# Kernel tuning notes

Measured on AMD Instinct MI355X. Metric: run time of the kernel, lower is better.

The kernel has to match this reference:

```python
import jax, jax.numpy as jnp
import numpy as np
import math

N_ATOMS = 128
BATCH = 8
FEAT = 64
K_BASIS = 16
N_IRR = 9            # (max_degree+1)^2 with max_degree=2
CUTOFF = 5.0
N_ELEM = 119
SQ3 = 1.7320508075688772

# degree of each of the 9 irrep components: l = 0,1,1,1,2,2,2,2,2
DEG = np.array([0, 1, 1, 1, 2, 2, 2, 2, 2])
_BINOM = jnp.asarray([math.comb(K_BASIS - 1, k) for k in range(K_BASIS)], dtype=jnp.float32)
_KPOW = jnp.arange(K_BASIS, dtype=jnp.float32)


def _sph(u):
    # real spherical harmonics up to l=2 of unit vectors u: [E,3] -> [E,9]
    ux, uy, uz = u[:, 0], u[:, 1], u[:, 2]
    return jnp.stack([
        jnp.ones_like(ux),
        ux, uy, uz,
        SQ3 * ux * uy, SQ3 * uy * uz, 0.5 * (3.0 * uz * uz - 1.0),
        SQ3 * ux * uz, 0.5 * SQ3 * (ux * ux - uy * uy),
    ], axis=-1)


def _basis(disp):
    # disp: [E,3] -> basis [E, 9, K]: Y_lm(u) * reciprocal-Bernstein radial * smooth cutoff
    r = jnp.sqrt(jnp.sum(disp * disp, axis=-1) + 1e-12)      # [E]
    Y = _sph(disp / r[:, None])                              # [E,9]
    w = 1.0 / (1.0 + r)                                      # reciprocal mapping to (0,1]
    rad = _BINOM * w[:, None] ** _KPOW * (1.0 - w)[:, None] ** (K_BASIS - 1.0 - _KPOW)  # [E,K]
    t = (r / CUTOFF) ** 2
    cut = jnp.where(t < 1.0, jnp.exp(1.0 - 1.0 / jnp.maximum(1.0 - t, 1e-12)), 0.0)     # [E]
    return Y[:, :, None] * (rad * cut[:, None])[:, None, :]


def _energy_single(z, pos, embed, WA, WB, W1, b1, W2, W1s, b1s, W2s, w_out, element_bias, dst, src):
    n = pos.shape[0]
    disp = pos[src] - pos[dst]                               # [E,3]
    B = _basis(disp)                                         # [E,9,K]
    # embed atomic numbers into the scalar (l=0) channel
    x = jnp.zeros((n, N_IRR, FEAT), pos.dtype).at[:, 0, :].set(embed[z])
    for i in range(2):  # full-degree message-passing iterations
        xs = x[src]                                          # gather  [E,9,F]
        # equivariant product paths: (scalar src) x (tensor basis) and (tensor src) x (scalar basis)
        mA = jnp.einsum('elk,kf,ef->elf', B, WA[i], xs[:, 0, :])
        mB = xs * jnp.einsum('ek,kf->ef', B[:, 0, :], WB[i])[:, None, :]
        y = jax.ops.segment_sum(mA + mB, dst, num_segments=n)  # scatter-add [N,9,F]
        y = x + y
        y = jnp.einsum('nlf,lfg->nlg', y, W1[i][DEG]).at[:, 0, :].add(b1[i])  # per-degree Dense
        s = y[:, 0, :]
        y = jnp.concatenate([jax.nn.silu(s)[:, None, :],
                             y[:, 1:, :] * jax.nn.sigmoid(s)[:, None, :]], axis=1)  # gated silu
        y = jnp.einsum('nlf,lfg->nlg', y, W2[i][DEG])
        x = x + y
    # last iteration: degree-0 output only (invariant contraction of all degrees)
    xs = x[src]
    mA = jnp.einsum('ek,kf,ef->ef', B[:, 0, :], WA[2], xs[:, 0, :])
    mB = jnp.einsum('elk,elf,kf->ef', B, xs, WB[2])
    y = jax.ops.segment_sum(mA + mB, dst, num_segments=n)    # [N,F]
    x0 = x[:, 0, :]
    h = x0 + y
    h = jax.nn.silu(h @ W1s + b1s) @ W2s
    x0 = x0 + h
    atomic_energies = x0 @ w_out + element_bias[z]           # [N]
    return jnp.sum(atomic_energies)


def setup_inputs() -> dict:
    ks = jax.random.split(jax.random.key(0), 16)
    ii, jj = np.meshgrid(np.arange(N_ATOMS), np.arange(N_ATOMS), indexing='ij')
    mask = ii != jj
    s = 1.0 / np.sqrt(FEAT)
    return {
        'features': jax.random.randint(ks[0], (BATCH, N_ATOMS), 1, N_ELEM, dtype=jnp.int32),
        'positions': jax.random.uniform(ks[1], (BATCH, N_ATOMS, 3), jnp.float32) * 12.0,
        'embed': 0.5 * jax.random.normal(ks[2], (N_ELEM, FEAT), jnp.float32),
        'WA': 0.1 * jax.random.normal(ks[3], (3, K_BASIS, FEAT), jnp.float32),
        'WB': 0.1 * jax.random.normal(ks[4], (3, K_BASIS, FEAT), jnp.float32),
        'W1': s * jax.random.normal(ks[5], (2, 3, FEAT, FEAT), jnp.float32),
        'b1': jnp.zeros((2, FEAT), jnp.float32),
        'W2': 0.1 * s * jax.random.normal(ks[6], (2, 3, FEAT, FEAT), jnp.float32),
        'W1s': s * jax.random.normal(ks[7], (FEAT, FEAT), jnp.float32),
        'b1s': jnp.zeros((FEAT,), jnp.float32),
        'W2s': 0.1 * s * jax.random.normal(ks[8], (FEAT, FEAT), jnp.float32),
        'w_out': 0.1 * jax.random.normal(ks[9], (FEAT,), jnp.float32),
        'element_bias': 0.01 * jax.random.normal(ks[10], (N_ELEM,), jnp.float32),
        'dst_idx': jnp.asarray(ii[mask], jnp.int32),
        'src_idx': jnp.asarray(jj[mask], jnp.int32),
    }


def reference(features, positions, embed, WA, WB, W1, b1, W2, W1s, b1s, W2s, w_out, element_bias, dst_idx, src_idx):
    params = (embed, WA, WB, W1, b1, W2, W1s, b1s, W2s, w_out, element_bias)

    def per_sample(z, pos):
        E, g = jax.value_and_grad(
            lambda p: _energy_single(z, p, *params, dst_idx, src_idx))(pos)
        return E, -g  # energy, forces = -dE/dpos

    return jax.vmap(per_sample)(features, positions)
```

## Files before the change

### kernel.cpp

```cpp
#include <hip/hip_runtime.h>
#include <math.h>

namespace {

constexpr int F   = 64;
constexpr int NA  = 128;
constexpr int NB  = 8;
constexpr int EPN = NA*(NA-1);
constexpr int K   = 16;
constexpr int L   = 9;
constexpr int BE  = NB*EPN;
constexpr int NNLF= NB*NA*L*F;
constexpr int BNF = NB*NA*F;
constexpr int GSP = 4;
constexpr int NSUB= 32;
constexpr float SQ3 = 1.7320508075688772f;

__device__ __constant__ float BINOM[16] = {1.f,15.f,105.f,455.f,1365.f,3003.f,5005.f,6435.f,
                                           6435.f,5005.f,3003.f,1365.f,455.f,105.f,15.f,1.f};
__device__ __constant__ int DEGC[9] = {0,1,1,1,2,2,2,2,2};

__device__ inline float wred(float v){
  #pragma unroll
  for (int o=32;o>0;o>>=1) v += __shfl_xor(v, o, 64);
  return v;
}

__device__ inline float qreduce(float v0, float v1, float v2, float v3, int lane){
  float a = ((lane&1)? v1 : v0) + __shfl_xor(((lane&1)? v0 : v1), 1, 64);
  float b = ((lane&1)? v3 : v2) + __shfl_xor(((lane&1)? v2 : v3), 1, 64);
  float r = ((lane&2)? b : a) + __shfl_xor(((lane&2)? a : b), 2, 64);
  r += __shfl_xor(r, 4, 64);
  r += __shfl_xor(r, 8, 64);
  r += __shfl_xor(r,16, 64);
  r += __shfl_xor(r,32, 64);
  return r;
}

__global__ void k_prep(const float* W1, const float* W2, const float* W1s,
                       const float* W2s, const float* wout,
                       float* W1T, float* W2T, float* W1sT, float* dsp,
                       float* outbuf){
  int idx = blockIdx.x*256 + threadIdx.x;
  if (idx < 6*F*F){
    int rem = idx % (F*F); int m = idx/(F*F); int g = rem/F, f = rem%F;
    W1T[idx] = W1[(m*F+f)*F+g];
    W2T[idx] = W2[(m*F+f)*F+g];
  } else if (idx < 6*F*F + F*F){
    int rem = idx - 6*F*F; int g = rem/F, f = rem%F;
    W1sT[rem] = W1s[f*F+g];
  } else if (idx < 6*F*F + F*F + F){
    int f = idx - 6*F*F - F*F;
    float s=0.f;
    for (int g=0; g<F; g++) s += W2s[f*F+g]*wout[g];
    dsp[f]=s;
  } else if (idx < 6*F*F + F*F + F + NB + NB*NA*3){
    outbuf[idx - (6*F*F + F*F + F)] = 0.f;
  }
}

__global__ void k_geom(const float* __restrict__ pos, const int* __restrict__ dsti,
                       const int* __restrict__ srci,
                       float* __restrict__ U, float* __restrict__ Rr,
                       float* __restrict__ Rp){
  int idx = blockIdx.x*256 + threadIdx.x;
  if (idx >= BE) return;
  int b = idx / EPN, e = idx % EPN;
  int d = dsti[e], s = srci[e];
  const float* pb = pos + (size_t)b*NA*3;
  float dx = pb[s*3+0]-pb[d*3+0];
  float dy = pb[s*3+1]-pb[d*3+1];
  float dz = pb[s*3+2]-pb[d*3+2];
  float ss = dx*dx+dy*dy+dz*dz + 1e-12f;
  float r  = sqrtf(ss);
  float ir = 1.f/r;
  U[(size_t)idx*4+0]=dx*ir; U[(size_t)idx*4+1]=dy*ir;
  U[(size_t)idx*4+2]=dz*ir; U[(size_t)idx*4+3]=ir;
  float w = 1.f/(1.f+r), v = 1.f - w;
  float wp[16], vp[16];
  wp[0]=1.f; vp[0]=1.f;
  #pragma unroll
  for (int k=1;k<16;k++){ wp[k]=wp[k-1]*w; vp[k]=vp[k-1]*v; }
  float t = (r*0.2f)*(r*0.2f);
  float cut=0.f, dcut=0.f;
  if (t < 1.f){
    float e1 = 1.f - t;
    float m  = fmaxf(e1, 1e-12f);
    cut = expf(1.f - 1.f/m);
    if (e1 > 1e-12f) dcut = -cut/(e1*e1) * (2.f*r*0.04f);
  }
  float nww = -w*w;
  #pragma unroll
  for (int k=0;k<16;k++){
    float rad = BINOM[k]*wp[k]*vp[15-k];
    float t1 = (k>0)  ? (float)k      * wp[k-1]*vp[15-k] : 0.f;
    float t2 = (k<15) ? (float)(15-k) * wp[k]  *vp[14-k] : 0.f;
    float dradr = BINOM[k]*(t1-t2)*nww;
    Rr[(size_t)idx*16+k] = rad*cut;
    Rp[(size_t)idx*16+k] = dradr*cut + rad*dcut;
  }
}

__global__ void k_init_x(const int* __restrict__ z, const float* __restrict__ embed,
                         float* __restrict__ x0){
  int b = blockIdx.x / NA, n = blockIdx.x % NA, f = threadIdx.x;
  int zi = z[b*NA+n];
  float* row = x0 + ((size_t)(b*NA+n))*L*F;
  row[f] = embed[(size_t)zi*F+f];
  #pragma unroll
  for (int l=1;l<L;l++) row[l*F+f]=0.f;
}

__global__ __launch_bounds__(64,4) void k_edge_fwd(const float* __restrict__ x,
    const float* __restrict__ WA, const float* __restrict__ WB,
    const float* __restrict__ U, const float* __restrict__ Rr,
    float* __restrict__ aggP){
  int bid = blockIdx.x;
  int g = bid & (GSP-1), bn = bid >> 2;
  int b = bn >> 7, n = bn & (NA-1);
  int f = threadIdx.x;
  float wa[K], wb[K];
  #pragma unroll
  for (int k=0;k<K;k++){ wa[k]=WA[k*F+f]; wb[k]=WB[k*F+f]; }
  float acc[L];
  #pragma unroll
  for (int l=0;l<L;l++) acc[l]=0.f;
  const float* xb = x + (size_t)b*NA*L*F;
  int c0 = g*NSUB, c1 = min(c0+NSUB, NA-1);
  #pragma unroll 2
  for (int c=c0; c<c1; ++c){
    int e = n*(NA-1)+c;
    int j = c + (c>=n);
    size_t ge = (size_t)b*EPN + e;
    const float* Re = Rr + ge*K;
    float RA=0.f, RB=0.f;
    #pragma unroll
    for (int k=0;k<K;k++){ float rk=Re[k]; RA += rk*wa[k]; RB += rk*wb[k]; }
    float ux=U[ge*4+0], uy=U[ge*4+1], uz=U[ge*4+2];
    float Y4=SQ3*ux*uy, Y5=SQ3*uy*uz, Y6=0.5f*(3.f*uz*uz-1.f);
    float Y7=SQ3*ux*uz, Y8=0.5f*SQ3*(ux*ux-uy*uy);
    const float* xr = xb + (size_t)j*L*F + f;
    float xs0 = xr[0];
    float t1 = RA*xs0;
    acc[0] += t1 + xs0*RB;
    acc[1] += ux*t1 + xr[1*F]*RB;
    acc[2] += uy*t1 + xr[2*F]*RB;
    acc[3] += uz*t1 + xr[3*F]*RB;
    acc[4] += Y4*t1 + xr[4*F]*RB;
    acc[5] += Y5*t1 + xr[5*F]*RB;
    acc[6] += Y6*t1 + xr[6*F]*RB;
    acc[7] += Y7*t1 + xr[7*F]*RB;
    acc[8] += Y8*t1 + xr[8*F]*RB;
  }
  float* ar = aggP + (size_t)g*NNLF + (size_t)bn*L*F + f;
  #pragma unroll
  for (int l=0;l<L;l++) ar[l*F] = acc[l];
}

__global__ __launch_bounds__(64) void k_node_fwd(const float* __restrict__ x,
    const float* __restrict__ aggP, const float* __restrict__ W1,
    const float* __restrict__ b1, const float* __restrict__ W2,
    float* __restrict__ y2out, float* __restrict__ xout){
  __shared__ float sh[L][F];
  int b = blockIdx.x / NA, n = blockIdx.x % NA, g = threadIdx.x;
  size_t base = ((size_t)(b*NA+n))*L*F;
  #pragma unroll
  for (int l=0;l<L;l++)
    sh[l][g] = x[base+l*F+g] + aggP[base+l*F+g] + aggP[NNLF+base+l*F+g]
             + aggP[2*(size_t)NNLF+base+l*F+g] + aggP[3*(size_t)NNLF+base+l*F+g];
  __syncthreads();
  float y2[L];
  #pragma unroll
  for (int l=0;l<L;l++){
    const float* W = W1 + DEGC[l]*F*F;
    float s=0.f;
    for (int ff=0; ff<F; ff++) s += sh[l][ff]*W[ff*F+g];
    y2[l]=s;
  }
  y2[0] += b1[g];
  #pragma unroll
  for (int l=0;l<L;l++) y2out[base+l*F+g] = y2[l];
  float sv = y2[0];
  float sg = 1.f/(1.f+expf(-sv));
  __syncthreads();
  sh[0][g] = sv*sg;
  #pragma unroll
  for (int l=1;l<L;l++) sh[l][g] = y2[l]*sg;
  __syncthreads();
  #pragma unroll
  for (int l=0;l<L;l++){
    const float* W = W2 + DEGC[l]*F*F;
    float s=0.f;
    for (int ff=0; ff<F; ff++) s += sh[l][ff]*W[ff*F+g];
    xout[base+l*F+g] = x[base+l*F+g] + s;
  }
}

__global__ __launch_bounds__(64,4) void k_redge_fwd(const float* __restrict__ x2,
    const float* __restrict__ WA2, const float* __restrict__ WB2,
    const float* __restrict__ U, const float* __restrict__ Rr,
    float* __restrict__ yRp){
  int bid = blockIdx.x;
  int g = bid & (GSP-1), bn = bid >> 2;
  int b = bn >> 7, n = bn & (NA-1);
  int f = threadIdx.x;
  float wa[K], wb[K];
  #pragma unroll
  for (int k=0;k<K;k++){ wa[k]=WA2[k*F+f]; wb[k]=WB2[k*F+f]; }
  float acc=0.f;
  const float* xb = x2 + (size_t)b*NA*L*F;
  int c0 = g*NSUB, c1 = min(c0+NSUB, NA-1);
  #pragma unroll 2
  for (int c=c0; c<c1; ++c){
    int e = n*(NA-1)+c;
    int j = c + (c>=n);
    size_t ge = (size_t)b*EPN + e;
    const float* Re = Rr + ge*K;
    float RA=0.f, RB=0.f;
    #pragma unroll
    for (int k=0;k<K;k++){ float rk=Re[k]; RA += rk*wa[k]; RB += rk*wb[k]; }
    float ux=U[ge*4+0], uy=U[ge*4+1], uz=U[ge*4+2];
    const float* xr = xb + (size_t)j*L*F + f;
    float xs0 = xr[0];
    float T = xs0
            + ux*xr[1*F] + uy*xr[2*F] + uz*xr[3*F]
            + (SQ3*ux*uy)*xr[4*F] + (SQ3*uy*uz)*xr[5*F]
            + (0.5f*(3.f*uz*uz-1.f))*xr[6*F]
            + (SQ3*ux*uz)*xr[7*F] + (0.5f*SQ3*(ux*ux-uy*uy))*xr[8*F];
    acc += RA*xs0 + RB*T;
  }
  yRp[(size_t)g*BNF + (size_t)bn*F + f] = acc;
}

__global__ __launch_bounds__(64) void k_rnode_fwd(const int* __restrict__ z,
    const float* __restrict__ x2, const float* __restrict__ yRp,
    const float* __restrict__ W1s, const float* __restrict__ b1s,
    const float* __restrict__ W2s, const float* __restrict__ wout,
    const float* __restrict__ ebias, float* __restrict__ pW, float* Eout){
  __shared__ float sh[F];
  int b = blockIdx.x / NA, n = blockIdx.x % NA, g = threadIdx.x;
  size_t base = ((size_t)(b*NA+n))*L*F;
  size_t nb   = (size_t)(b*NA+n)*F;
  float x0 = x2[base+g];
  sh[g] = x0 + yRp[nb+g] + yRp[BNF+nb+g] + yRp[2*(size_t)BNF+nb+g] + yRp[3*(size_t)BNF+nb+g];
  __syncthreads();
  float p = b1s[g];
  for (int ff=0; ff<F; ff++) p += sh[ff]*W1s[ff*F+g];
  pW[nb+g] = p;
  float sp = p/(1.f+expf(-p));
  __syncthreads();
  sh[g] = sp;
  __syncthreads();
  float h2=0.f;
  for (int ff=0; ff<F; ff++) h2 += sh[ff]*W2s[ff*F+g];
  float xo = x0 + h2;
  float en = wred(xo*wout[g]);
  if (g==0) atomicAdd(Eout+b, en + ebias[z[b*NA+n]]);
}

__global__ __launch_bounds__(64) void k_rnode_bwd(const float* __restrict__ pW,
    const float* __restrict__ dsp, const float* __restrict__ W1sT,
    const float* __restrict__ wout, float* __restrict__ dyR, float* __restrict__ dxA){
  __shared__ float sh[F];
  int b = blockIdx.x / NA, n = blockIdx.x % NA, f = threadIdx.x;
  size_t nb = (size_t)(b*NA+n)*F;
  float p  = pW[nb+f];
  float sg = 1.f/(1.f+expf(-p));
  float dp = dsp[f]*sg*(1.f + p*(1.f-sg));
  sh[f]=dp;
  __syncthreads();
  float dh1=0.f;
  for (int g=0; g<F; g++) dh1 += sh[g]*W1sT[g*F+f];
  dyR[nb+f]=dh1;
  size_t base = ((size_t)(b*NA+n))*L*F;
  dxA[base+f] = wout[f]+dh1;
  #pragma unroll
  for (int l=1;l<L;l++) dxA[base+l*F+f]=0.f;
}

__global__ __launch_bounds__(64,4) void k_redge_bwd(const float* __restrict__ x2,
    const float* __restrict__ WA2, const float* __restrict__ WB2,
    const float* __restrict__ U, const float* __restrict__ Rr,
    const float* __restrict__ Rp, const float* __restrict__ dyR,
    float* __restrict__ partP, float* Fout){
  int bid = blockIdx.x;
  int g = bid & (GSP-1), bn = bid >> 2;
  int b = bn >> 7, j = bn & (NA-1);
  int f = threadIdx.x, m = f & 3;
  float wa[K], wb[K];
  #pragma unroll
  for (int k=0;k<K;k++){ wa[k]=WA2[k*F+f]; wb[k]=WB2[k*F+f]; }
  size_t xbase = ((size_t)bn)*L*F;
  float xs[L];
  #pragma unroll
  for (int l=0;l<L;l++) xs[l]=x2[xbase+l*F+f];
  float acc[L];
  #pragma unroll
  for (int l=0;l<L;l++) acc[l]=0.f;
  float sdd=0.f;
  int i0 = g*NSUB, i1 = min(i0+NSUB, NA-1);
  for (int ii=i0; ii<i1; ++ii){
    int i = ii + (ii>=j);
    int c = (j<i)? j : j-1;
    size_t ge = (size_t)b*EPN + i*(NA-1)+c;
    float gv = dyR[(size_t)(b*NA+i)*F+f];
    const float* Re = Rr + ge*K;
    const float* Pe = Rp + ge*K;
    float RA=0.f,RB=0.f,PA=0.f,PB=0.f;
    #pragma unroll
    for (int k=0;k<K;k++){ float rk=Re[k],pk=Pe[k];
      RA+=rk*wa[k]; RB+=rk*wb[k]; PA+=pk*wa[k]; PB+=pk*wb[k]; }
    float ux=U[ge*4+0], uy=U[ge*4+1], uz=U[ge*4+2], ir=U[ge*4+3];
    float Y4=SQ3*ux*uy, Y5=SQ3*uy*uz, Y6=0.5f*(3.f*uz*uz-1.f);
    float Y7=SQ3*ux*uz, Y8=0.5f*SQ3*(ux*ux-uy*uy);
    float T = xs[0] + ux*xs[1]+uy*xs[2]+uz*xs[3]
            + Y4*xs[4]+Y5*xs[5]+Y6*xs[6]+Y7*xs[7]+Y8*xs[8];
    float X0 = xs[1] + SQ3*(uy*xs[4]+uz*xs[7]+ux*xs[8]);
    float X1 = xs[2] + SQ3*(ux*xs[4]+uz*xs[5]-uy*xs[8]);
    float X2 = xs[3] + SQ3*(uy*xs[5]+ux*xs[7]) + 3.f*uz*xs[6];
    acc[0] += gv*(RA+RB);
    acc[1] += gv*ux*RB; acc[2] += gv*uy*RB; acc[3] += gv*uz*RB;
    acc[4] += gv*Y4*RB; acc[5] += gv*Y5*RB; acc[6] += gv*Y6*RB;
    acc[7] += gv*Y7*RB; acc[8] += gv*Y8*RB;
    float gRB = gv*RB;
    float r4 = qreduce(gRB*X0, gRB*X1, gRB*X2, gv*(xs[0]*PA + T*PB), f);
    float um = (m==0)?ux : (m==1)?uy : (m==2)?uz : 0.f;
    float q = r4*um;
    q += __shfl_xor(q,1,64); q += __shfl_xor(q,2,64);
    float SR = __shfl(r4, f|3, 64);
    float dd = (r4 - q*um)*ir + SR*um;
    if (f<3) atomicAdd(&Fout[(size_t)(b*NA+i)*3+f], dd);
    sdd += dd;
  }
  float* ar = partP + (size_t)g*NNLF + xbase + f;
  #pragma unroll
  for (int l=0;l<L;l++) ar[l*F] = acc[l];
  if (f<3) atomicAdd(&Fout[(size_t)(b*NA+j)*3+f], -sdd);
}

template<bool WDX>
__global__ __launch_bounds__(64) void k_node_bwd(const float* __restrict__ dxIn,
    const float* __restrict__ partP, const float* __restrict__ y2W,
    const float* __restrict__ W1T, const float* __restrict__ W2T,
    float* __restrict__ dagg, float* __restrict__ dxOut){
  __shared__ float A[L][F];
  __shared__ float Bb[L][F];
  int f = threadIdx.x;
  size_t base = ((size_t)blockIdx.x)*L*F;
  #pragma unroll
  for (int l=0;l<L;l++)
    A[l][f] = dxIn[base+l*F+f] + partP[base+l*F+f] + partP[NNLF+base+l*F+f]
            + partP[2*(size_t)NNLF+base+l*F+f] + partP[3*(size_t)NNLF+base+l*F+f];
  __syncthreads();
  float dy3[L];
  #pragma unroll
  for (int l=0;l<L;l++){
    const float* W = W2T + DEGC[l]*F*F;
    float s=0.f;
    for (int g=0; g<F; g++) s += A[l][g]*W[g*F+f];
    dy3[l]=s;
  }
  float sv = y2W[base+f];
  float sg = 1.f/(1.f+expf(-sv));
  float ds = dy3[0]*sg*(1.f+sv*(1.f-sg));
  float dy2[L];
  #pragma unroll
  for (int l=1;l<L;l++){
    float y2l = y2W[base+l*F+f];
    ds += dy3[l]*y2l*sg*(1.f-sg);
    dy2[l] = dy3[l]*sg;
  }
  dy2[0]=ds;
  #pragma unroll
  for (int l=0;l<L;l++) Bb[l][f]=dy2[l];
  __syncthreads();
  #pragma unroll
  for (int l=0;l<L;l++){
    const float* W = W1T + DEGC[l]*F*F;
    float s=0.f;
    for (int g=0; g<F; g++) s += Bb[l][g]*W[g*F+f];
    dagg[base+l*F+f]=s;
    if (WDX) dxOut[base+l*F+f] = A[l][f] + s;
  }
}

template<bool WDX>
__global__ __launch_bounds__(64,4) void k_edge_bwd(const float* __restrict__ xI,
    const float* __restrict__ WA, const float* __restrict__ WB,
    const float* __restrict__ U, const float* __restrict__ Rr,
    const float* __restrict__ Rp, const float* __restrict__ dagg,
    float* __restrict__ partP, float* Fout){
  int bid = blockIdx.x;
  int g = bid & (GSP-1), bn = bid >> 2;
  int b = bn >> 7, j = bn & (NA-1);
  int f = threadIdx.x, m = f & 3;
  float wa[K], wb[K];
  #pragma unroll
  for (int k=0;k<K;k++){ wa[k]=WA[k*F+f]; wb[k]=WB[k*F+f]; }
  size_t xbase = ((size_t)bn)*L*F;
  float xs[L];
  #pragma unroll
  for (int l=0;l<L;l++) xs[l]=xI[xbase+l*F+f];
  float acc[L]; float acc0=0.f;
  #pragma unroll
  for (int l=0;l<L;l++) acc[l]=0.f;
  float sdd=0.f;
  int i0 = g*NSUB, i1 = min(i0+NSUB, NA-1);
  for (int ii=i0; ii<i1; ++ii){
    int i = ii + (ii>=j);
    int c = (j<i)? j : j-1;
    size_t ge = (size_t)b*EPN + i*(NA-1)+c;
    const float* gr = dagg + ((size_t)(b*NA+i))*L*F + f;
    float gl[L];
    #pragma unroll
    for (int l=0;l<L;l++) gl[l]=gr[l*F];
    const float* Re = Rr + ge*K;
    const float* Pe = Rp + ge*K;
    float RA=0.f,RB=0.f,PA=0.f,PB=0.f;
    #pragma unroll
    for (int k=0;k<K;k++){ float rk=Re[k],pk=Pe[k];
      RA+=rk*wa[k]; RB+=rk*wb[k]; PA+=pk*wa[k]; PB+=pk*wb[k]; }
    float ux=U[ge*4+0], uy=U[ge*4+1], uz=U[ge*4+2], ir=U[ge*4+3];
    float Y4=SQ3*ux*uy, Y5=SQ3*uy*uz, Y6=0.5f*(3.f*uz*uz-1.f);
    float Y7=SQ3*ux*uz, Y8=0.5f*SQ3*(ux*ux-uy*uy);
    float gy = gl[0] + gl[1]*ux+gl[2]*uy+gl[3]*uz
             + gl[4]*Y4+gl[5]*Y5+gl[6]*Y6+gl[7]*Y7+gl[8]*Y8;
    float gx = 0.f;
    #pragma unroll
    for (int l=0;l<L;l++) gx += gl[l]*xs[l];
    float G0 = gl[1] + SQ3*(uy*gl[4]+uz*gl[7]+ux*gl[8]);
    float G1 = gl[2] + SQ3*(ux*gl[4]+uz*gl[5]-uy*gl[8]);
    float G2 = gl[3] + SQ3*(uy*gl[5]+ux*gl[7]) + 3.f*uz*gl[6];
    if (WDX){
      acc0 += gy*RA;
      #pragma unroll
      for (int l=0;l<L;l++) acc[l] += gl[l]*RB;
    }
    float cm = RA*xs[0];
    float r4 = qreduce(cm*G0, cm*G1, cm*G2, gy*xs[0]*PA + gx*PB, f);
    float um = (m==0)?ux : (m==1)?uy : (m==2)?uz : 0.f;
    float q = r4*um;
    q += __shfl_xor(q,1,64); q += __shfl_xor(q,2,64);
    float SR = __shfl(r4, f|3, 64);
    float dd = (r4 - q*um)*ir + SR*um;
    if (f<3) atomicAdd(&Fout[(size_t)(b*NA+i)*3+f], dd);
    sdd += dd;
  }
  if (WDX){
    float* ar = partP + (size_t)g*NNLF + xbase + f;
    ar[0] = acc0 + acc[0];
    #pragma unroll
    for (int l=1;l<L;l++) ar[l*F] = acc[l];
  }
  if (f<3) atomicAdd(&Fout[(size_t)(b*NA+j)*3+f], -sdd);
}

}

extern "C" void kernel_launch(void* const* d_in, const int* in_sizes, int n_in,
                              void* d_out, int out_size, void* d_ws, size_t ws_size,
                              hipStream_t stream){
  (void)in_sizes; (void)n_in; (void)out_size; (void)ws_size;
  const int*   z     = (const int*)  d_in[0];
  const float* pos   = (const float*)d_in[1];
  const float* emb   = (const float*)d_in[2];
  const float* WA    = (const float*)d_in[3];
  const float* WB    = (const float*)d_in[4];
  const float* W1    = (const float*)d_in[5];
  const float* b1    = (const float*)d_in[6];
  const float* W2    = (const float*)d_in[7];
  const float* W1s   = (const float*)d_in[8];
  const float* b1s   = (const float*)d_in[9];
  const float* W2s   = (const float*)d_in[10];
  const float* wout  = (const float*)d_in[11];
  const float* ebias = (const float*)d_in[12];
  const int*   dsti  = (const int*)  d_in[13];
  const int*   srci  = (const int*)  d_in[14];

  float* w    = (float*)d_ws;
  float* U    = w;
  float* Rr   = U    + (size_t)BE*4;
  float* Rp   = Rr   + (size_t)BE*16;
  float* x0   = Rp   + (size_t)BE*16;
  float* x1   = x0   + NNLF;
  float* x2   = x1   + NNLF;
  float* y2b  = x2   + NNLF;
  float* part = y2b  + 2*(size_t)NNLF;
  float* yRp  = part + 4*(size_t)NNLF;
  float* pW   = yRp  + 4*(size_t)BNF;
  float* dyR  = pW   + BNF;
  float* dxA  = dyR  + BNF;
  float* dxO  = dxA  + NNLF;
  float* dagg = dxO  + NNLF;
  float* W1T  = dagg + NNLF;
  float* W2T  = W1T  + 6*F*F;
  float* W1sT = W2T  + 6*F*F;
  float* dspv = W1sT + F*F;

  float* Eout = (float*)d_out;
  float* Fout = Eout + NB;

  dim3 bn(NB*NA);
  dim3 be(NB*NA*GSP);

  k_prep  <<<126, 256, 0, stream>>>(W1, W2, W1s, W2s, wout, W1T, W2T, W1sT, dspv, Eout);
  k_geom  <<<(BE+255)/256, 256, 0, stream>>>(pos, dsti, srci, U, Rr, Rp);
  k_init_x<<<bn, 64, 0, stream>>>(z, emb, x0);

  k_edge_fwd<<<be, 64, 0, stream>>>(x0, WA,     WB,     U, Rr, part);
  k_node_fwd<<<bn, 64, 0, stream>>>(x0, part, W1,       b1,   W2,       y2b,      x1);
  k_edge_fwd<<<be, 64, 0, stream>>>(x1, WA+K*F, WB+K*F, U, Rr, part);
  k_node_fwd<<<bn, 64, 0, stream>>>(x1, part, W1+3*F*F, b1+F, W2+3*F*F, y2b+NNLF, x2);
  k_redge_fwd<<<be, 64, 0, stream>>>(x2, WA+2*K*F, WB+2*K*F, U, Rr, yRp);
  k_rnode_fwd<<<bn, 64, 0, stream>>>(z, x2, yRp, W1s, b1s, W2s, wout, ebias, pW, Eout);

  k_rnode_bwd<<<bn, 64, 0, stream>>>(pW, dspv, W1sT, wout, dyR, dxA);
  k_redge_bwd<<<be, 64, 0, stream>>>(x2, WA+2*K*F, WB+2*K*F, U, Rr, Rp, dyR, part, Fout);
  k_node_bwd<true ><<<bn, 64, 0, stream>>>(dxA, part, y2b+NNLF, W1T+3*F*F, W2T+3*F*F, dagg, dxO);
  k_edge_bwd<true ><<<be, 64, 0, stream>>>(x1, WA+K*F, WB+K*F, U, Rr, Rp, dagg, part, Fout);
  k_node_bwd<false><<<bn, 64, 0, stream>>>(dxO, part, y2b, W1T, W2T, dagg, nullptr);
  k_edge_bwd<false><<<be, 64, 0, stream>>>(x0, WA, WB, U, Rr, Rp, dagg, nullptr, Fout);
}
```

Before: 402.5 us.

## Split edge loops finer, widen node kernels, pack weights, skip zero channels

Doubles the number of edge-loop splits (GSP 8, NSUB 16) so more wavefronts run in parallel. Node kernels go from 64 to 256 threads, with the irrep rows or matmul slices spread across four waves. Radial weight pairs are packed into float2 vectors so the compiler can emit packed FMAs. First-layer kernels skip the l>0 source channels, which are known to be zero from the embedding. In exchange there are more partial-sum buffers to reduce and higher launch-bounds occupancy targets, which may cause register spills.

```diff
diff --git a/kernel.cpp b/kernel.cpp
--- a/kernel.cpp
+++ b/kernel.cpp
@@ -12,9 +12,11 @@
 constexpr int BE  = NB*EPN;
 constexpr int NNLF= NB*NA*L*F;
 constexpr int BNF = NB*NA*F;
-constexpr int GSP = 4;
-constexpr int NSUB= 32;
+constexpr int GSP = 8;
+constexpr int NSUB= 16;
 constexpr float SQ3 = 1.7320508075688772f;
+
+typedef float v2f __attribute__((ext_vector_type(2)));
 
 __device__ __constant__ float BINOM[16] = {1.f,15.f,105.f,455.f,1365.f,3003.f,5005.f,6435.f,
                                            6435.f,5005.f,3003.f,1365.f,455.f,105.f,15.f,1.f};
@@ -111,17 +113,18 @@
   for (int l=1;l<L;l++) row[l*F+f]=0.f;
 }
 
-__global__ __launch_bounds__(64,4) void k_edge_fwd(const float* __restrict__ x,
+template<bool FIRST>
+__global__ __launch_bounds__(64,6) void k_edge_fwd(const float* __restrict__ x,
     const float* __restrict__ WA, const float* __restrict__ WB,
     const float* __restrict__ U, const float* __restrict__ Rr,
     float* __restrict__ aggP){
   int bid = blockIdx.x;
-  int g = bid & (GSP-1), bn = bid >> 2;
+  int g = bid & (GSP-1), bn = bid >> 3;
   int b = bn >> 7, n = bn & (NA-1);
   int f = threadIdx.x;
-  float wa[K], wb[K];
-  #pragma unroll
-  for (int k=0;k<K;k++){ wa[k]=WA[k*F+f]; wb[k]=WB[k*F+f]; }
+  v2f wab[K];
+  #pragma unroll
+  for (int k=0;k<K;k++){ v2f t = {WA[k*F+f], WB[k*F+f]}; wab[k]=t; }
   float acc[L];
   #pragma unroll
   for (int l=0;l<L;l++) acc[l]=0.f;
@@ -133,9 +136,10 @@
     int j = c + (c>=n);
     size_t ge = (size_t)b*EPN + e;
     const float* Re = Rr + ge*K;
-    float RA=0.f, RB=0.f;
-    #pragma unroll
-    for (int k=0;k<K;k++){ float rk=Re[k]; RA += rk*wa[k]; RB += rk*wb[k]; }
+    v2f AB = {0.f, 0.f};
+    #pragma unroll
+    for (int k=0;k<K;k++) AB += Re[k]*wab[k];
+    float RA=AB.x, RB=AB.y;
     float ux=U[ge*4+0], uy=U[ge*4+1], uz=U[ge*4+2];
     float Y4=SQ3*ux*uy, Y5=SQ3*uy*uz, Y6=0.5f*(3.f*uz*uz-1.f);
     float Y7=SQ3*ux*uz, Y8=0.5f*SQ3*(ux*ux-uy*uy);
@@ -143,70 +147,75 @@
     float xs0 = xr[0];
     float t1 = RA*xs0;
     acc[0] += t1 + xs0*RB;
-    acc[1] += ux*t1 + xr[1*F]*RB;
-    acc[2] += uy*t1 + xr[2*F]*RB;
-    acc[3] += uz*t1 + xr[3*F]*RB;
-    acc[4] += Y4*t1 + xr[4*F]*RB;
-    acc[5] += Y5*t1 + xr[5*F]*RB;
-    acc[6] += Y6*t1 + xr[6*F]*RB;
-    acc[7] += Y7*t1 + xr[7*F]*RB;
-    acc[8] += Y8*t1 + xr[8*F]*RB;
+    if (FIRST){
+      acc[1] += ux*t1; acc[2] += uy*t1; acc[3] += uz*t1;
+      acc[4] += Y4*t1; acc[5] += Y5*t1; acc[6] += Y6*t1;
+      acc[7] += Y7*t1; acc[8] += Y8*t1;
+    } else {
+      acc[1] += ux*t1 + xr[1*F]*RB;
+      acc[2] += uy*t1 + xr[2*F]*RB;
+      acc[3] += uz*t1 + xr[3*F]*RB;
+      acc[4] += Y4*t1 + xr[4*F]*RB;
+      acc[5] += Y5*t1 + xr[5*F]*RB;
+      acc[6] += Y6*t1 + xr[6*F]*RB;
+      acc[7] += Y7*t1 + xr[7*F]*RB;
+      acc[8] += Y8*t1 + xr[8*F]*RB;
+    }
   }
   float* ar = aggP + (size_t)g*NNLF + (size_t)bn*L*F + f;
   #pragma unroll
   for (int l=0;l<L;l++) ar[l*F] = acc[l];
 }
 
-__global__ __launch_bounds__(64) void k_node_fwd(const float* __restrict__ x,
+__global__ __launch_bounds__(256) void k_node_fwd(const float* __restrict__ x,
     const float* __restrict__ aggP, const float* __restrict__ W1,
     const float* __restrict__ b1, const float* __restrict__ W2,
     float* __restrict__ y2out, float* __restrict__ xout){
-  __shared__ float sh[L][F];
-  int b = blockIdx.x / NA, n = blockIdx.x % NA, g = threadIdx.x;
-  size_t base = ((size_t)(b*NA+n))*L*F;
-  #pragma unroll
-  for (int l=0;l<L;l++)
-    sh[l][g] = x[base+l*F+g] + aggP[base+l*F+g] + aggP[NNLF+base+l*F+g]
-             + aggP[2*(size_t)NNLF+base+l*F+g] + aggP[3*(size_t)NNLF+base+l*F+g];
-  __syncthreads();
-  float y2[L];
-  #pragma unroll
-  for (int l=0;l<L;l++){
-    const float* W = W1 + DEGC[l]*F*F;
+  __shared__ float sh[L*F];
+  __shared__ float yb[L*F];
+  __shared__ float zb[L*F];
+  int t = threadIdx.x, g = t&63, w = t>>6;
+  size_t base = ((size_t)blockIdx.x)*L*F;
+  for (int idx=t; idx<L*F; idx+=256){
+    float s = x[base+idx];
+    #pragma unroll
+    for (int sl=0; sl<GSP; sl++) s += aggP[(size_t)sl*NNLF + base + idx];
+    sh[idx]=s;
+  }
+  __syncthreads();
+  for (int l=w; l<L; l+=4){
+    const float* W = W1 + DEGC[l]*F*F + g;
     float s=0.f;
-    for (int ff=0; ff<F; ff++) s += sh[l][ff]*W[ff*F+g];
-    y2[l]=s;
-  }
-  y2[0] += b1[g];
-  #pragma unroll
-  for (int l=0;l<L;l++) y2out[base+l*F+g] = y2[l];
-  float sv = y2[0];
+    for (int ff=0; ff<F; ff++) s += sh[l*F+ff]*W[(size_t)ff*F];
+    if (l==0) s += b1[g];
+    y2out[base+l*F+g]=s;
+    yb[l*F+g]=s;
+  }
+  __syncthreads();
+  float sv = yb[g];
   float sg = 1.f/(1.f+expf(-sv));
-  __syncthreads();
-  sh[0][g] = sv*sg;
-  #pragma unroll
-  for (int l=1;l<L;l++) sh[l][g] = y2[l]*sg;
-  __syncthreads();
-  #pragma unroll
-  for (int l=0;l<L;l++){
-    const float* W = W2 + DEGC[l]*F*F;
+  for (int l=w; l<L; l+=4)
+    zb[l*F+g] = (l==0)? sv*sg : yb[l*F+g]*sg;
+  __syncthreads();
+  for (int l=w; l<L; l+=4){
+    const float* W = W2 + DEGC[l]*F*F + g;
     float s=0.f;
-    for (int ff=0; ff<F; ff++) s += sh[l][ff]*W[ff*F+g];
+    for (int ff=0; ff<F; ff++) s += zb[l*F+ff]*W[(size_t)ff*F];
     xout[base+l*F+g] = x[base+l*F+g] + s;
   }
 }
 
-__global__ __launch_bounds__(64,4) void k_redge_fwd(const float* __restrict__ x2,
+__global__ __launch_bounds__(64,6) void k_redge_fwd(const float* __restrict__ x2,
     const float* __restrict__ WA2, const float* __restrict__ WB2,
     const float* __restrict__ U, const float* __restrict__ Rr,
     float* __restrict__ yRp){
   int bid = blockIdx.x;
-  int g = bid & (GSP-1), bn = bid >> 2;
+  int g = bid & (GSP-1), bn = bid >> 3;
   int b = bn >> 7, n = bn & (NA-1);
   int f = threadIdx.x;
-  float wa[K], wb[K];
-  #pragma unroll
-  for (int k=0;k<K;k++){ wa[k]=WA2[k*F+f]; wb[k]=WB2[k*F+f]; }
+  v2f wab[K];
+  #pragma unroll
+  for (int k=0;k<K;k++){ v2f t = {WA2[k*F+f], WB2[k*F+f]}; wab[k]=t; }
   float acc=0.f;
   const float* xb = x2 + (size_t)b*NA*L*F;
   int c0 = g*NSUB, c1 = min(c0+NSUB, NA-1);
@@ -216,9 +225,10 @@
     int j = c + (c>=n);
     size_t ge = (size_t)b*EPN + e;
     const float* Re = Rr + ge*K;
-    float RA=0.f, RB=0.f;
-    #pragma unroll
-    for (int k=0;k<K;k++){ float rk=Re[k]; RA += rk*wa[k]; RB += rk*wb[k]; }
+    v2f AB = {0.f, 0.f};
+    #pragma unroll
+    for (int k=0;k<K;k++) AB += Re[k]*wab[k];
+    float RA=AB.x, RB=AB.y;
     float ux=U[ge*4+0], uy=U[ge*4+1], uz=U[ge*4+2];
     const float* xr = xb + (size_t)j*L*F + f;
     float xs0 = xr[0];
@@ -232,64 +242,85 @@
   yRp[(size_t)g*BNF + (size_t)bn*F + f] = acc;
 }
 
-__global__ __launch_bounds__(64) void k_rnode_fwd(const int* __restrict__ z,
+__global__ __launch_bounds__(256) void k_rnode_fwd(const int* __restrict__ z,
     const float* __restrict__ x2, const float* __restrict__ yRp,
     const float* __restrict__ W1s, const float* __restrict__ b1s,
     const float* __restrict__ W2s, const float* __restrict__ wout,
     const float* __restrict__ ebias, float* __restrict__ pW, float* Eout){
   __shared__ float sh[F];
-  int b = blockIdx.x / NA, n = blockIdx.x % NA, g = threadIdx.x;
-  size_t base = ((size_t)(b*NA+n))*L*F;
-  size_t nb   = (size_t)(b*NA+n)*F;
-  float x0 = x2[base+g];
-  sh[g] = x0 + yRp[nb+g] + yRp[BNF+nb+g] + yRp[2*(size_t)BNF+nb+g] + yRp[3*(size_t)BNF+nb+g];
-  __syncthreads();
-  float p = b1s[g];
-  for (int ff=0; ff<F; ff++) p += sh[ff]*W1s[ff*F+g];
-  pW[nb+g] = p;
+  __shared__ float part[4][F];
+  int t = threadIdx.x, g = t&63, w = t>>6;
+  int bnn = blockIdx.x;
+  int b = bnn >> 7;
+  size_t base = (size_t)bnn*L*F;
+  size_t nb   = (size_t)bnn*F;
+  if (t < F){
+    float s = x2[base+t];
+    #pragma unroll
+    for (int sl=0; sl<GSP; sl++) s += yRp[(size_t)sl*BNF + nb + t];
+    sh[t]=s;
+  }
+  __syncthreads();
+  float pp=0.f;
+  for (int ff=w*16; ff<w*16+16; ff++) pp += sh[ff]*W1s[(size_t)ff*F+g];
+  part[w][g]=pp;
+  __syncthreads();
+  float p = part[0][g]+part[1][g]+part[2][g]+part[3][g] + b1s[g];
+  if (w==0) pW[nb+g]=p;
   float sp = p/(1.f+expf(-p));
   __syncthreads();
-  sh[g] = sp;
-  __syncthreads();
-  float h2=0.f;
-  for (int ff=0; ff<F; ff++) h2 += sh[ff]*W2s[ff*F+g];
-  float xo = x0 + h2;
-  float en = wred(xo*wout[g]);
-  if (g==0) atomicAdd(Eout+b, en + ebias[z[b*NA+n]]);
-}
-
-__global__ __launch_bounds__(64) void k_rnode_bwd(const float* __restrict__ pW,
+  if (w==0) sh[g]=sp;
+  __syncthreads();
+  float h=0.f;
+  for (int ff=w*16; ff<w*16+16; ff++) h += sh[ff]*W2s[(size_t)ff*F+g];
+  part[w][g]=h;
+  __syncthreads();
+  if (w==0){
+    float h2 = part[0][g]+part[1][g]+part[2][g]+part[3][g];
+    float x0v = x2[base+g];
+    float en = wred((x0v+h2)*wout[g]);
+    if (g==0) atomicAdd(Eout+b, en + ebias[z[bnn]]);
+  }
+}
+
+__global__ __launch_bounds__(256) void k_rnode_bwd(const float* __restrict__ pW,
     const float* __restrict__ dsp, const float* __restrict__ W1sT,
     const float* __restrict__ wout, float* __restrict__ dyR, float* __restrict__ dxA){
   __shared__ float sh[F];
-  int b = blockIdx.x / NA, n = blockIdx.x % NA, f = threadIdx.x;
-  size_t nb = (size_t)(b*NA+n)*F;
-  float p  = pW[nb+f];
-  float sg = 1.f/(1.f+expf(-p));
-  float dp = dsp[f]*sg*(1.f + p*(1.f-sg));
-  sh[f]=dp;
-  __syncthreads();
-  float dh1=0.f;
-  for (int g=0; g<F; g++) dh1 += sh[g]*W1sT[g*F+f];
-  dyR[nb+f]=dh1;
-  size_t base = ((size_t)(b*NA+n))*L*F;
-  dxA[base+f] = wout[f]+dh1;
-  #pragma unroll
-  for (int l=1;l<L;l++) dxA[base+l*F+f]=0.f;
-}
-
-__global__ __launch_bounds__(64,4) void k_redge_bwd(const float* __restrict__ x2,
+  __shared__ float part[4][F];
+  int t = threadIdx.x, g = t&63, w = t>>6;
+  size_t nb = (size_t)blockIdx.x*F;
+  size_t base = (size_t)blockIdx.x*L*F;
+  if (t < F){
+    float p  = pW[nb+t];
+    float sgm = 1.f/(1.f+expf(-p));
+    sh[t] = dsp[t]*sgm*(1.f + p*(1.f-sgm));
+  }
+  __syncthreads();
+  float s=0.f;
+  for (int ff=w*16; ff<w*16+16; ff++) s += sh[ff]*W1sT[(size_t)ff*F+g];
+  part[w][g]=s;
+  __syncthreads();
+  if (w==0){
+    float dh1 = part[0][g]+part[1][g]+part[2][g]+part[3][g];
+    dyR[nb+g]=dh1;
+    dxA[base+g] = wout[g]+dh1;
+  }
+  for (int idx=t; idx<(L-1)*F; idx+=256) dxA[base+F+idx]=0.f;
+}
+
+__global__ __launch_bounds__(64,6) void k_redge_bwd(const float* __restrict__ x2,
     const float* __restrict__ WA2, const float* __restrict__ WB2,
     const float* __restrict__ U, const float* __restrict__ Rr,
     const float* __restrict__ Rp, const float* __restrict__ dyR,
     float* __restrict__ partP, float* Fout){
   int bid = blockIdx.x;
-  int g = bid & (GSP-1), bn = bid >> 2;
+  int g = bid & (GSP-1), bn = bid >> 3;
   int b = bn >> 7, j = bn & (NA-1);
   int f = threadIdx.x, m = f & 3;
-  float wa[K], wb[K];
-  #pragma unroll
-  for (int k=0;k<K;k++){ wa[k]=WA2[k*F+f]; wb[k]=WB2[k*F+f]; }
+  v2f wab[K];
+  #pragma unroll
+  for (int k=0;k<K;k++){ v2f t = {WA2[k*F+f], WB2[k*F+f]}; wab[k]=t; }
   size_t xbase = ((size_t)bn)*L*F;
   float xs[L];
   #pragma unroll
@@ -299,6 +330,7 @@
   for (int l=0;l<L;l++) acc[l]=0.f;
   float sdd=0.f;
   int i0 = g*NSUB, i1 = min(i0+NSUB, NA-1);
+  #pragma unroll 2
   for (int ii=i0; ii<i1; ++ii){
     int i = ii + (ii>=j);
     int c = (j<i)? j : j-1;
@@ -306,10 +338,10 @@
     float gv = dyR[(size_t)(b*NA+i)*F+f];
     const float* Re = Rr + ge*K;
     const float* Pe = Rp + ge*K;
-    float RA=0.f,RB=0.f,PA=0.f,PB=0.f;
-    #pragma unroll
-    for (int k=0;k<K;k++){ float rk=Re[k],pk=Pe[k];
-      RA+=rk*wa[k]; RB+=rk*wb[k]; PA+=pk*wa[k]; PB+=pk*wb[k]; }
+    v2f RAB = {0.f,0.f}, PAB = {0.f,0.f};
+    #pragma unroll
+    for (int k=0;k<K;k++){ RAB += Re[k]*wab[k]; PAB += Pe[k]*wab[k]; }
+    float RA=RAB.x, RB=RAB.y, PA=PAB.x, PB=PAB.y;
     float ux=U[ge*4+0], uy=U[ge*4+1], uz=U[ge*4+2], ir=U[ge*4+3];
     float Y4=SQ3*ux*uy, Y5=SQ3*uy*uz, Y6=0.5f*(3.f*uz*uz-1.f);
     float Y7=SQ3*ux*uz, Y8=0.5f*SQ3*(ux*ux-uy*uy);
@@ -339,73 +371,79 @@
 }
 
 template<bool WDX>
-__global__ __launch_bounds__(64) void k_node_bwd(const float* __restrict__ dxIn,
+__global__ __launch_bounds__(256) void k_node_bwd(const float* __restrict__ dxIn,
     const float* __restrict__ partP, const float* __restrict__ y2W,
     const float* __restrict__ W1T, const float* __restrict__ W2T,
     float* __restrict__ dagg, float* __restrict__ dxOut){
-  __shared__ float A[L][F];
-  __shared__ float Bb[L][F];
-  int f = threadIdx.x;
+  __shared__ float A[L*F];
+  __shared__ float D3[L*F];
+  __shared__ float Bb[L*F];
+  __shared__ float prt[4][F];
+  int t = threadIdx.x, g = t&63, w = t>>6;
   size_t base = ((size_t)blockIdx.x)*L*F;
-  #pragma unroll
-  for (int l=0;l<L;l++)
-    A[l][f] = dxIn[base+l*F+f] + partP[base+l*F+f] + partP[NNLF+base+l*F+f]
-            + partP[2*(size_t)NNLF+base+l*F+f] + partP[3*(size_t)NNLF+base+l*F+f];
-  __syncthreads();
-  float dy3[L];
-  #pragma unroll
-  for (int l=0;l<L;l++){
-    const float* W = W2T + DEGC[l]*F*F;
+  for (int idx=t; idx<L*F; idx+=256){
+    float s = dxIn[base+idx];
+    #pragma unroll
+    for (int sl=0; sl<GSP; sl++) s += partP[(size_t)sl*NNLF + base + idx];
+    A[idx]=s;
+  }
+  __syncthreads();
+  float pc=0.f;
+  for (int l=w; l<L; l+=4){
+    const float* W = W2T + DEGC[l]*F*F + g;
     float s=0.f;
-    for (int g=0; g<F; g++) s += A[l][g]*W[g*F+f];
-    dy3[l]=s;
-  }
-  float sv = y2W[base+f];
+    for (int ff=0; ff<F; ff++) s += A[l*F+ff]*W[(size_t)ff*F];
+    D3[l*F+g]=s;
+    if (l>0) pc += s * y2W[base+l*F+g];
+  }
+  prt[w][g]=pc;
+  __syncthreads();
+  float sv = y2W[base+g];
   float sg = 1.f/(1.f+expf(-sv));
-  float ds = dy3[0]*sg*(1.f+sv*(1.f-sg));
-  float dy2[L];
-  #pragma unroll
-  for (int l=1;l<L;l++){
-    float y2l = y2W[base+l*F+f];
-    ds += dy3[l]*y2l*sg*(1.f-sg);
-    dy2[l] = dy3[l]*sg;
-  }
-  dy2[0]=ds;
-  #pragma unroll
-  for (int l=0;l<L;l++) Bb[l][f]=dy2[l];
-  __syncthreads();
-  #pragma unroll
-  for (int l=0;l<L;l++){
-    const float* W = W1T + DEGC[l]*F*F;
+  for (int l=w; l<L; l+=4){
+    float v;
+    if (l==0){
+      float sum = prt[0][g]+prt[1][g]+prt[2][g]+prt[3][g];
+      v = D3[g]*sg*(1.f+sv*(1.f-sg)) + sum*sg*(1.f-sg);
+    } else {
+      v = D3[l*F+g]*sg;
+    }
+    Bb[l*F+g]=v;
+  }
+  __syncthreads();
+  for (int l=w; l<L; l+=4){
+    const float* W = W1T + DEGC[l]*F*F + g;
     float s=0.f;
-    for (int g=0; g<F; g++) s += Bb[l][g]*W[g*F+f];
-    dagg[base+l*F+f]=s;
-    if (WDX) dxOut[base+l*F+f] = A[l][f] + s;
-  }
-}
-
-template<bool WDX>
-__global__ __launch_bounds__(64,4) void k_edge_bwd(const float* __restrict__ xI,
+    for (int ff=0; ff<F; ff++) s += Bb[l*F+ff]*W[(size_t)ff*F];
+    dagg[base+l*F+g]=s;
+    if (WDX) dxOut[base+l*F+g] = A[l*F+g] + s;
+  }
+}
+
+template<bool WDX, bool FIRST>
+__global__ __launch_bounds__(64,6) void k_edge_bwd(const float* __restrict__ xI,
     const float* __restrict__ WA, const float* __restrict__ WB,
     const float* __restrict__ U, const float* __restrict__ Rr,
     const float* __restrict__ Rp, const float* __restrict__ dagg,
     float* __restrict__ partP, float* Fout){
   int bid = blockIdx.x;
-  int g = bid & (GSP-1), bn = bid >> 2;
+  int g = bid & (GSP-1), bn = bid >> 3;
   int b = bn >> 7, j = bn & (NA-1);
   int f = threadIdx.x, m = f & 3;
-  float wa[K], wb[K];
-  #pragma unroll
-  for (int k=0;k<K;k++){ wa[k]=WA[k*F+f]; wb[k]=WB[k*F+f]; }
+  v2f wab[K];
+  #pragma unroll
+  for (int k=0;k<K;k++){ v2f t = {WA[k*F+f], WB[k*F+f]}; wab[k]=t; }
   size_t xbase = ((size_t)bn)*L*F;
   float xs[L];
-  #pragma unroll
-  for (int l=0;l<L;l++) xs[l]=xI[xbase+l*F+f];
+  xs[0] = xI[xbase+f];
+  #pragma unroll
+  for (int l=1;l<L;l++) xs[l] = FIRST ? 0.f : xI[xbase+l*F+f];
   float acc[L]; float acc0=0.f;
   #pragma unroll
   for (int l=0;l<L;l++) acc[l]=0.f;
   float sdd=0.f;
   int i0 = g*NSUB, i1 = min(i0+NSUB, NA-1);
+  #pragma unroll 2
   for (int ii=i0; ii<i1; ++ii){
     int i = ii + (ii>=j);
     int c = (j<i)? j : j-1;
@@ -416,18 +454,23 @@
     for (int l=0;l<L;l++) gl[l]=gr[l*F];
     const float* Re = Rr + ge*K;
     const float* Pe = Rp + ge*K;
-    float RA=0.f,RB=0.f,PA=0.f,PB=0.f;
-    #pragma unroll
-    for (int k=0;k<K;k++){ float rk=Re[k],pk=Pe[k];
-      RA+=rk*wa[k]; RB+=rk*wb[k]; PA+=pk*wa[k]; PB+=pk*wb[k]; }
+    v2f RAB = {0.f,0.f}, PAB = {0.f,0.f};
+    #pragma unroll
+    for (int k=0;k<K;k++){ RAB += Re[k]*wab[k]; PAB += Pe[k]*wab[k]; }
+    float RA=RAB.x, RB=RAB.y, PA=PAB.x, PB=PAB.y;
     float ux=U[ge*4+0], uy=U[ge*4+1], uz=U[ge*4+2], ir=U[ge*4+3];
     float Y4=SQ3*ux*uy, Y5=SQ3*uy*uz, Y6=0.5f*(3.f*uz*uz-1.f);
     float Y7=SQ3*ux*uz, Y8=0.5f*SQ3*(ux*ux-uy*uy);
     float gy = gl[0] + gl[1]*ux+gl[2]*uy+gl[3]*uz
              + gl[4]*Y4+gl[5]*Y5+gl[6]*Y6+gl[7]*Y7+gl[8]*Y8;
-    float gx = 0.f;
-    #pragma unroll
-    for (int l=0;l<L;l++) gx += gl[l]*xs[l];
+    float gx;
+    if (FIRST){
+      gx = gl[0]*xs[0];
+    } else {
+      gx = 0.f;
+      #pragma unroll
+      for (int l=0;l<L;l++) gx += gl[l]*xs[l];
+    }
     float G0 = gl[1] + SQ3*(uy*gl[4]+uz*gl[7]+ux*gl[8]);
     float G1 = gl[2] + SQ3*(ux*gl[4]+uz*gl[5]-uy*gl[8]);
     float G2 = gl[3] + SQ3*(uy*gl[5]+ux*gl[7]) + 3.f*uz*gl[6];
@@ -486,8 +529,8 @@
   float* x2   = x1   + NNLF;
   float* y2b  = x2   + NNLF;
   float* part = y2b  + 2*(size_t)NNLF;
-  float* yRp  = part + 4*(size_t)NNLF;
-  float* pW   = yRp  + 4*(size_t)BNF;
+  float* yRp  = part + (size_t)GSP*NNLF;
+  float* pW   = yRp  + (size_t)GSP*BNF;
   float* dyR  = pW   + BNF;
   float* dxA  = dyR  + BNF;
   float* dxO  = dxA  + NNLF;
@@ -507,17 +550,17 @@
   k_geom  <<<(BE+255)/256, 256, 0, stream>>>(pos, dsti, srci, U, Rr, Rp);
   k_init_x<<<bn, 64, 0, stream>>>(z, emb, x0);
 
-  k_edge_fwd<<<be, 64, 0, stream>>>(x0, WA,     WB,     U, Rr, part);
-  k_node_fwd<<<bn, 64, 0, stream>>>(x0, part, W1,       b1,   W2,       y2b,      x1);
-  k_edge_fwd<<<be, 64, 0, stream>>>(x1, WA+K*F, WB+K*F, U, Rr, part);
-  k_node_fwd<<<bn, 64, 0, stream>>>(x1, part, W1+3*F*F, b1+F, W2+3*F*F, y2b+NNLF, x2);
+  k_edge_fwd<true ><<<be, 64, 0, stream>>>(x0, WA,     WB,     U, Rr, part);
+  k_node_fwd<<<bn, 256, 0, stream>>>(x0, part, W1,       b1,   W2,       y2b,      x1);
+  k_edge_fwd<false><<<be, 64, 0, stream>>>(x1, WA+K*F, WB+K*F, U, Rr, part);
+  k_node_fwd<<<bn, 256, 0, stream>>>(x1, part, W1+3*F*F, b1+F, W2+3*F*F, y2b+NNLF, x2);
   k_redge_fwd<<<be, 64, 0, stream>>>(x2, WA+2*K*F, WB+2*K*F, U, Rr, yRp);
-  k_rnode_fwd<<<bn, 64, 0, stream>>>(z, x2, yRp, W1s, b1s, W2s, wout, ebias, pW, Eout);
-
-  k_rnode_bwd<<<bn, 64, 0, stream>>>(pW, dspv, W1sT, wout, dyR, dxA);
+  k_rnode_fwd<<<bn, 256, 0, stream>>>(z, x2, yRp, W1s, b1s, W2s, wout, ebias, pW, Eout);
+
+  k_rnode_bwd<<<bn, 256, 0, stream>>>(pW, dspv, W1sT, wout, dyR, dxA);
   k_redge_bwd<<<be, 64, 0, stream>>>(x2, WA+2*K*F, WB+2*K*F, U, Rr, Rp, dyR, part, Fout);
-  k_node_bwd<true ><<<bn, 64, 0, stream>>>(dxA, part, y2b+NNLF, W1T+3*F*F, W2T+3*F*F, dagg, dxO);
-  k_edge_bwd<true ><<<be, 64, 0, stream>>>(x1, WA+K*F, WB+K*F, U, Rr, Rp, dagg, part, Fout);
-  k_node_bwd<false><<<bn, 64, 0, stream>>>(dxO, part, y2b, W1T, W2T, dagg, nullptr);
-  k_edge_bwd<false><<<be, 64, 0, stream>>>(x0, WA, WB, U, Rr, Rp, dagg, nullptr, Fout);
-}
+  k_node_bwd<true ><<<bn, 256, 0, stream>>>(dxA, part, y2b+NNLF, W1T+3*F*F, W2T+3*F*F, dagg, dxO);
+  k_edge_bwd<true ,false><<<be, 64, 0, stream>>>(x1, WA+K*F, WB+K*F, U, Rr, Rp, dagg, part, Fout);
+  k_node_bwd<false><<<bn, 256, 0, stream>>>(dxO, part, y2b, W1T, W2T, dagg, nullptr);
+  k_edge_bwd<false,true ><<<be, 64, 0, stream>>>(x0, WA, WB, U, Rr, Rp, dagg, nullptr, Fout);
+}
```

Measured after the change: 421.7 us. 4.8% more time.
